# Optimization experiments

Hardware: AMD Instinct MI355X
Metric: run time of the kernel (lower is better)

The kernel has to match this reference:

```python
import jax, jax.numpy as jnp
import numpy as np

BLOCK = 32
LAYER_MAX = 6.0
E2M1_BOUNDS = jnp.array([0.25, 0.75, 1.25, 1.75, 2.5, 3.5, 5.0], dtype=jnp.float32)
E2M1_VALUES = jnp.array([0.0, 0.5, 1.0, 1.5, 2.0, 3.0, 4.0, 6.0], dtype=jnp.float32)


def setup_inputs() -> dict:
    key = jax.random.key(0)
    k1, k2 = jax.random.split(key)
    out_f, in_f = 8192, 8192
    num_blocks = out_f * (in_f // BLOCK)
    weight_fp = jax.random.normal(k1, (out_f, in_f), dtype=jnp.float32) * 0.05
    # eps_param is the learned pre-tanh block offset (one scalar per block)
    eps_param = jax.random.normal(k2, (num_blocks,), dtype=jnp.float32) * 0.2
    return {"weight_fp": weight_fp, "eps_param": eps_param}


def reference(weight_fp, eps_param):
    out_f, in_f = weight_fp.shape
    nb = in_f // BLOCK
    # [out_f, nb, BLOCK]
    w_blocks = weight_fp.reshape(out_f, nb, BLOCK)
    amax = jnp.max(jnp.abs(w_blocks), axis=-1, keepdims=True)
    descale = amax / LAYER_MAX
    # e8m0 scale: exp2(ceil(max(log2(descale), -127)))
    e8m0_scale = jnp.ceil(jnp.maximum(jnp.log2(descale), -127.0))
    scale = jnp.exp2(e8m0_scale)  # [out_f, nb, 1]
    w_norm = w_blocks / scale
    # block epsilon offset: eps = 0.5 * tanh(p) in (-0.5, 0.5)
    eps_base = 0.5 * jnp.tanh(eps_param)  # [out_f*nb]
    eps_blocks = eps_base.reshape(out_f, nb, 1)
    abs_shifted = jnp.maximum(jnp.abs(w_norm) + eps_blocks, 0.0)
    sign = jnp.sign(w_norm)
    # matches torch (2 - sign) // 2 : 0 for positive, 1 for negative/zero
    sign_bit = jnp.floor((2.0 - sign) / 2.0)
    # threshold-count encode against E2M1 bounds -> ord in [0, 7]
    ord_ = jnp.sum(abs_shifted[..., None] > E2M1_BOUNDS, axis=-1)  # int32 [out_f, nb, BLOCK]
    encoded = (sign_bit.astype(jnp.int32) * 8 + ord_).astype(jnp.uint8)
    # dequantize via values-table gather
    mantissa = E2M1_VALUES[ord_]
    signed_mantissa = mantissa * (1.0 - 2.0 * sign_bit)
    deq_weight = (signed_mantissa * scale).reshape(out_f, in_f)
    e8m0_scale_uint8 = (e8m0_scale + 127.0).astype(jnp.uint8)  # [out_f, nb, 1]
    return (deq_weight, encoded.reshape(out_f, in_f), e8m0_scale_uint8, eps_base)
```

## Files before the change

kernel.cpp:

```cpp
#include <hip/hip_runtime.h>
#include <math.h>


constexpr long long OUT_F = 8192;
constexpr long long IN_F  = 8192;
constexpr long long NELEM = OUT_F * IN_F;
constexpr long long NBLK  = NELEM / 32;

__global__ __launch_bounds__(256) void e2m1_quant_kernel(
    const float* __restrict__ w,
    const float* __restrict__ eps_p,
    float* __restrict__ out)
{
    const long long tid  = (long long)blockIdx.x * blockDim.x + threadIdx.x;
    const long long b    = tid >> 3;
    const int       sub  = (int)(tid & 7);
    const long long base = b * 32 + (long long)sub * 4;

    const float4 wv = *reinterpret_cast<const float4*>(w + base);

    float a = fmaxf(fmaxf(fabsf(wv.x), fabsf(wv.y)),
                    fmaxf(fabsf(wv.z), fabsf(wv.w)));
    a = fmaxf(a, __shfl_xor(a, 1));
    a = fmaxf(a, __shfl_xor(a, 2));
    a = fmaxf(a, __shfl_xor(a, 4));

    const float descale = a * (1.0f / 6.0f) ;
    const float descale_div = a / 6.0f;
    float lf = __log2f(descale_div);
    (void)descale;
    lf = fmaxf(lf, -127.0f);
    const float e8 = ceilf(lf);
    const int   ei = (int)e8;
    const float rscale = ldexpf(1.0f, -ei);

    const float p  = eps_p[b];
    const float t  = fabsf(p);
    const float em = __expf(-2.0f * t);
    const float th = (1.0f - em) / (1.0f + em);
    const float ep = 0.5f * copysignf(th, p);

    const float vals[4] = {wv.x, wv.y, wv.z, wv.w};
    float deq[4], enc[4];

#pragma unroll
    for (int i = 0; i < 4; ++i) {
        const float wn = vals[i] * rscale;
        const float as = fmaxf(fabsf(wn) + ep, 0.0f);
        const int o = (as > 0.25f) + (as > 0.75f) + (as > 1.25f) + (as > 1.75f)
                    + (as > 2.5f)  + (as > 3.5f)  + (as > 5.0f);
        const int sbit = (wn <= 0.0f) ? 1 : 0;
        const float mant = (o < 2) ? (float)o * 0.5f
                                   : ldexpf(1.0f + (float)(o & 1) * 0.5f, (o >> 1) - 1);
        const float sgn = sbit ? -1.0f : 1.0f;
        deq[i] = ldexpf(mant * sgn, ei);
        enc[i] = (float)(sbit * 8 + o);
    }

    *reinterpret_cast<float4*>(out + base) =
        make_float4(deq[0], deq[1], deq[2], deq[3]);
    *reinterpret_cast<float4*>(out + NELEM + base) =
        make_float4(enc[0], enc[1], enc[2], enc[3]);

    if (sub == 0) {
        out[2 * NELEM + b]        = e8 + 127.0f;
        out[2 * NELEM + NBLK + b] = ep;
    }
}

extern "C" void kernel_launch(void* const* d_in, const int* in_sizes, int n_in,
                              void* d_out, int out_size, void* d_ws, size_t ws_size,
                              hipStream_t stream) {
    const float* w     = (const float*)d_in[0];
    const float* eps_p = (const float*)d_in[1];
    float* out = (float*)d_out;

    const long long n_threads = NELEM / 4;
    const int block = 256;
    const int grid  = (int)(n_threads / block);
    e2m1_quant_kernel<<<grid, block, 0, stream>>>(w, eps_p, out);
}
```

Measured before the change: 688.4 us.

## Process eight elements per thread with nontemporal vector loads and stores

Each thread now handles 8 elements, loaded as two f32x4 vectors, so four lanes cover one 32-element block instead of eight. That removes one shuffle stage and halves the number of threads. All global loads and stores of the weight, dequantized and encoded data use nontemporal builtins to limit cache pollution in this streaming kernel. Indexing switches to 32-bit unsigned arithmetic. The ALU work is also reduced: log2 plus ceil becomes exponent-bit manipulation, the tanh division becomes a hardware reciprocal, and the mantissa comes from a packed nibble lookup table.

```diff
diff --git a/kernel.cpp b/kernel.cpp
--- a/kernel.cpp
+++ b/kernel.cpp
@@ -2,68 +2,71 @@
 #include <math.h>
 
 
-constexpr long long OUT_F = 8192;
-constexpr long long IN_F  = 8192;
-constexpr long long NELEM = OUT_F * IN_F;
-constexpr long long NBLK  = NELEM / 32;
+typedef float f32x4 __attribute__((ext_vector_type(4)));
+
+constexpr unsigned long long NELEM = 8192ull * 8192ull;
+constexpr unsigned           NBLK  = (unsigned)(NELEM / 32);
 
 __global__ __launch_bounds__(256) void e2m1_quant_kernel(
     const float* __restrict__ w,
     const float* __restrict__ eps_p,
     float* __restrict__ out)
 {
-    const long long tid  = (long long)blockIdx.x * blockDim.x + threadIdx.x;
-    const long long b    = tid >> 3;
-    const int       sub  = (int)(tid & 7);
-    const long long base = b * 32 + (long long)sub * 4;
+    const unsigned tid  = blockIdx.x * 256u + threadIdx.x;
+    const unsigned b    = tid >> 2;
+    const unsigned sub  = tid & 3u;
+    const unsigned base = b * 32u + sub * 4u;
 
-    const float4 wv = *reinterpret_cast<const float4*>(w + base);
+    const f32x4* wp = reinterpret_cast<const f32x4*>(w + base);
+    const f32x4 w0 = __builtin_nontemporal_load(wp);
+    const f32x4 w1 = __builtin_nontemporal_load(wp + 4);
+    const float p  = eps_p[b];
 
-    float a = fmaxf(fmaxf(fabsf(wv.x), fabsf(wv.y)),
-                    fmaxf(fabsf(wv.z), fabsf(wv.w)));
+    float a = fmaxf(fmaxf(fmaxf(fabsf(w0[0]), fabsf(w0[1])),
+                          fmaxf(fabsf(w0[2]), fabsf(w0[3]))),
+                    fmaxf(fmaxf(fabsf(w1[0]), fabsf(w1[1])),
+                          fmaxf(fabsf(w1[2]), fabsf(w1[3]))));
     a = fmaxf(a, __shfl_xor(a, 1));
     a = fmaxf(a, __shfl_xor(a, 2));
-    a = fmaxf(a, __shfl_xor(a, 4));
 
-    const float descale = a * (1.0f / 6.0f) ;
-    const float descale_div = a / 6.0f;
-    float lf = __log2f(descale_div);
-    (void)descale;
-    lf = fmaxf(lf, -127.0f);
-    const float e8 = ceilf(lf);
-    const int   ei = (int)e8;
-    const float rscale = ldexpf(1.0f, -ei);
+    const float descale = a / 6.0f;
+    const unsigned du = __float_as_uint(descale);
+    const int ex = (int)(du >> 23);
+    int e = ex - 127 + ((du & 0x7fffffu) ? 1 : 0);
+    e = (ex == 0) ? -127 : e;
+    e = (e < -127) ? -127 : e;
+    const float rscale = ldexpf(1.0f, -e);
 
-    const float p  = eps_p[b];
     const float t  = fabsf(p);
     const float em = __expf(-2.0f * t);
-    const float th = (1.0f - em) / (1.0f + em);
+    const float th = (1.0f - em) * __builtin_amdgcn_rcpf(1.0f + em);
     const float ep = 0.5f * copysignf(th, p);
 
-    const float vals[4] = {wv.x, wv.y, wv.z, wv.w};
-    float deq[4], enc[4];
+    const float vals[8] = {w0[0], w0[1], w0[2], w0[3],
+                           w1[0], w1[1], w1[2], w1[3]};
+    float dq[8], ec[8];
 
 #pragma unroll
-    for (int i = 0; i < 4; ++i) {
+    for (int i = 0; i < 8; ++i) {
         const float wn = vals[i] * rscale;
         const float as = fmaxf(fabsf(wn) + ep, 0.0f);
         const int o = (as > 0.25f) + (as > 0.75f) + (as > 1.25f) + (as > 1.75f)
                     + (as > 2.5f)  + (as > 3.5f)  + (as > 5.0f);
-        const int sbit = (wn <= 0.0f) ? 1 : 0;
-        const float mant = (o < 2) ? (float)o * 0.5f
-                                   : ldexpf(1.0f + (float)(o & 1) * 0.5f, (o >> 1) - 1);
-        const float sgn = sbit ? -1.0f : 1.0f;
-        deq[i] = ldexpf(mant * sgn, ei);
-        enc[i] = (float)(sbit * 8 + o);
+        const bool neg = (wn <= 0.0f);
+        const int nib = (int)((0xC8643210u >> (o * 4)) & 0xFu);
+        dq[i] = ldexpf((float)(neg ? -nib : nib), e - 1);
+        ec[i] = (float)(o | (neg ? 8 : 0));
     }
 
-    *reinterpret_cast<float4*>(out + base) =
-        make_float4(deq[0], deq[1], deq[2], deq[3]);
-    *reinterpret_cast<float4*>(out + NELEM + base) =
-        make_float4(enc[0], enc[1], enc[2], enc[3]);
+    f32x4* dptr = reinterpret_cast<f32x4*>(out + base);
+    __builtin_nontemporal_store((f32x4){dq[0], dq[1], dq[2], dq[3]}, dptr);
+    __builtin_nontemporal_store((f32x4){dq[4], dq[5], dq[6], dq[7]}, dptr + 4);
+    f32x4* eptr = reinterpret_cast<f32x4*>(out + NELEM + base);
+    __builtin_nontemporal_store((f32x4){ec[0], ec[1], ec[2], ec[3]}, eptr);
+    __builtin_nontemporal_store((f32x4){ec[4], ec[5], ec[6], ec[7]}, eptr + 4);
 
     if (sub == 0) {
-        out[2 * NELEM + b]        = e8 + 127.0f;
+        out[2 * NELEM + b]        = (float)(e + 127);
         out[2 * NELEM + NBLK + b] = ep;
     }
 }
@@ -75,8 +78,8 @@
     const float* eps_p = (const float*)d_in[1];
     float* out = (float*)d_out;
 
-    const long long n_threads = NELEM / 4;
+    const unsigned n_threads = NBLK * 4u;
     const int block = 256;
-    const int grid  = (int)(n_threads / block);
+    const int grid  = (int)(n_threads / (unsigned)block);
     e2m1_quant_kernel<<<grid, block, 0, stream>>>(w, eps_p, out);
 }
```

New measurement: 706.4 us. 1.03x slower.
